# Kernel tuning notes

Measured on AMD Instinct MI355X. Metric: run time of the kernel, lower is better.

The kernel has to match this reference:

```python
import jax, jax.numpy as jnp
import numpy as np

N, E, D, H, LAYERS = 50000, 800000, 128, 8, 2
LRELU_ALPHA = 0.2


def _seg_softmax(logits, seg, n):
    # numerically stable softmax over edges grouped by destination node
    m = jax.ops.segment_max(logits, seg, num_segments=n)
    z = jnp.exp(logits - m[seg])
    s = jax.ops.segment_sum(z, seg, num_segments=n)
    return z / jnp.maximum(s[seg], 1e-16)


def _gat_layer(x, src, dst, W, a_src, a_dst, concat):
    # W: [H, Fin, F'], a_src/a_dst: [H, F']
    n = x.shape[0]
    outs = []
    for h in range(W.shape[0]):  # loop over heads to bound peak memory
        Wh = x @ W[h]                              # [N, F']
        es = Wh @ a_src[h]                         # [N]
        ed = Wh @ a_dst[h]                         # [N]
        e = jax.nn.leaky_relu(es[src] + ed[dst], LRELU_ALPHA)  # [E]
        att = _seg_softmax(e, dst, n)              # [E]
        out = jax.ops.segment_sum(att[:, None] * Wh[src], dst, num_segments=n)
        outs.append(out)
    if concat:
        return jax.nn.elu(jnp.concatenate(outs, axis=-1))  # [N, H*F']
    return jnp.mean(jnp.stack(outs, axis=0), axis=0)        # [N, F']


def _rel_gcn_layer(x, src, dst, w, W):
    # weighted-adjacency GCN with row (in-degree) normalization + ReLU
    n = x.shape[0]
    deg = jax.ops.segment_sum(w, dst, num_segments=n)
    norm = w / jnp.maximum(deg[dst], 1e-16)        # [E]
    h = x @ W                                      # [N, Dout]
    agg = jax.ops.segment_sum(norm[:, None] * h[src], dst, num_segments=n)
    return jax.nn.relu(agg)


def setup_inputs() -> dict:
    key = jax.random.key(0)
    ks = jax.random.split(key, 12)
    s = 1.0 / np.sqrt(D)
    return {
        "x": jax.random.normal(ks[0], (N, D), dtype=jnp.float32),
        "edge_index": jax.random.randint(ks[1], (2, E), 0, N, dtype=jnp.int64),
        "edge_weight": jax.random.uniform(ks[2], (E,), dtype=jnp.float32),
        "gat_W0": jax.random.normal(ks[3], (H, D, D // H), dtype=jnp.float32) * s,
        "gat_a0_src": jax.random.normal(ks[4], (H, D // H), dtype=jnp.float32) * s,
        "gat_a0_dst": jax.random.normal(ks[5], (H, D // H), dtype=jnp.float32) * s,
        "gat_W1": jax.random.normal(ks[6], (H, D, D), dtype=jnp.float32) * s,
        "gat_a1_src": jax.random.normal(ks[7], (H, D), dtype=jnp.float32) * s,
        "gat_a1_dst": jax.random.normal(ks[8], (H, D), dtype=jnp.float32) * s,
        "gcn_W0": jax.random.normal(ks[9], (D, D), dtype=jnp.float32) * s,
        "gcn_W1": jax.random.normal(ks[10], (D, D), dtype=jnp.float32) * s,
    }


def reference(x, edge_index, edge_weight, gat_W0, gat_a0_src, gat_a0_dst,
              gat_W1, gat_a1_src, gat_a1_dst, gcn_W0, gcn_W1):
    src, dst = edge_index[0], edge_index[1]
    gat_params = [(gat_W0, gat_a0_src, gat_a0_dst), (gat_W1, gat_a1_src, gat_a1_dst)]
    gcn_params = [gcn_W0, gcn_W1]
    x1, x2 = x, x  # dropout is identity in eval mode
    for i in range(LAYERS):
        W, a_s, a_d = gat_params[i]
        x1 = _gat_layer(x1, src, dst, W, a_s, a_d, concat=(i != LAYERS - 1))
        x2 = _rel_gcn_layer(x2, src, dst, edge_weight, gcn_params[i])
    # cat along new last dim then MaxPool1d(2) == elementwise max of branches
    return jnp.maximum(x1, x2)
```

## Files before the change

kernel.cpp:

```cpp
#include <hip/hip_runtime.h>

#define LRELU_ALPHA 0.2f

typedef __attribute__((ext_vector_type(8))) short short8;
typedef __attribute__((ext_vector_type(4))) float float4v;
typedef __attribute__((ext_vector_type(2))) float f32x2;

__device__ __forceinline__ unsigned short f2bf(float f) {
  union { float f; unsigned u; } x; x.f = f;
  unsigned r = (x.u + 0x7fff + ((x.u >> 16) & 1)) >> 16;
  return (unsigned short)r;
}
__device__ __forceinline__ float bflo(unsigned u) {
  union { unsigned u; float f; } x; x.u = u << 16; return x.f;
}
__device__ __forceinline__ float bfhi(unsigned u) {
  union { unsigned u; float f; } x; x.u = u & 0xffff0000u; return x.f;
}
__device__ __forceinline__ f32x2 bfpair(unsigned u) {
  return (f32x2){bflo(u), bfhi(u)};
}


__global__ __launch_bounds__(256) void k_count(const int* __restrict__ dst,
                                               int* __restrict__ cnt, int E) {
  int e = blockIdx.x * 256 + threadIdx.x;
  if (e < E) atomicAdd(&cnt[dst[e]], 1);
}

__global__ __launch_bounds__(1024) void k_scan1(const int* __restrict__ cnt,
                                                int* __restrict__ lscan,
                                                int* __restrict__ bsum, int N) {
  __shared__ int sm[1024];
  int t = threadIdx.x;
  int base = blockIdx.x * 1024;
  int v = (base + t < N) ? cnt[base + t] : 0;
  sm[t] = v;
  __syncthreads();
  for (int off = 1; off < 1024; off <<= 1) {
    int x = (t >= off) ? sm[t - off] : 0;
    __syncthreads();
    sm[t] += x;
    __syncthreads();
  }
  if (base + t < N) lscan[base + t] = sm[t] - v;
  if (t == 1023) bsum[blockIdx.x] = sm[1023];
}

__global__ __launch_bounds__(64) void k_scan2(int* __restrict__ bsum,
                                              int* __restrict__ rowptrN, int nb) {
  int t = threadIdx.x;
  int v = (t < nb) ? bsum[t] : 0;
  int orig = v;
  for (int off = 1; off < 64; off <<= 1) {
    int y = __shfl_up(v, off, 64);
    if (t >= off) v += y;
  }
  if (t < nb) bsum[t] = v - orig;
  if (t == 63) *rowptrN = v;
}

__global__ __launch_bounds__(1024) void k_scan3(int* __restrict__ rowptr,
                                                int* __restrict__ cur,
                                                const int* __restrict__ bsum, int N) {
  int i = blockIdx.x * 1024 + threadIdx.x;
  if (i < N) {
    int v = rowptr[i] + bsum[blockIdx.x];
    rowptr[i] = v;
    cur[i] = v;
  }
}

__global__ __launch_bounds__(256) void k_scatter(const int* __restrict__ src,
                                                 const int* __restrict__ dst,
                                                 const float* __restrict__ w,
                                                 int* __restrict__ cur,
                                                 uint2* __restrict__ edata, int E) {
  int e = blockIdx.x * 256 + threadIdx.x;
  if (e < E) {
    int d = dst[e];
    int p = atomicAdd(&cur[d], 1);
    edata[p] = make_uint2((unsigned)src[e], __float_as_uint(w[e]));
  }
}

__global__ __launch_bounds__(256) void k_pack(const float* __restrict__ W0,
                                              const float* __restrict__ a0s,
                                              const float* __restrict__ a0d,
                                              const float* __restrict__ W1,
                                              const float* __restrict__ a1s,
                                              const float* __restrict__ a1d,
                                              const float* __restrict__ gw0,
                                              const float* __restrict__ gw1,
                                              unsigned short* __restrict__ W0catT,
                                              float* __restrict__ logitW,
                                              unsigned short* __restrict__ gw1T,
                                              unsigned short* __restrict__ va1T,
                                              unsigned short* __restrict__ WstackT) {
  int idx = blockIdx.x * 256 + threadIdx.x;
  if (idx < 32768) {
    int n = idx >> 7, k = idx & 127;
    int q = n >> 2, r = n & 3;
    float v;
    if (r < 2) {
      int o = 2 * q + r;
      int h = o >> 4, f = o & 15;
      v = W0[h * 2048 + k * 16 + f];
    } else {
      int j = 2 * q + (r - 2);
      v = gw0[k * 128 + j];
    }
    W0catT[idx] = f2bf(v);
  } else if (idx < 34816) {
    int j = idx - 32768;
    int k = j >> 4, c = j & 15;
    int h = (c < 8) ? c : c - 8;
    const float* a = (c < 8) ? a0s : a0d;
    float s = 0.f;
    for (int f = 0; f < 16; ++f) s += W0[h * 2048 + k * 16 + f] * a[h * 16 + f];
    logitW[j] = s;
  } else if (idx < 51200) {
    int j = idx - 34816;
    int n = j >> 7, k = j & 127;
    gw1T[j] = f2bf(gw1[k * 128 + n]);
  } else if (idx < 53248) {
    int j = idx - 51200;
    int c = j >> 7, k = j & 127;
    int h = c & 7;
    const float* a = (c < 8) ? a1s : a1d;
    float s = 0.f;
    for (int f = 0; f < 128; ++f) s += W1[h * 16384 + k * 128 + f] * a[h * 128 + f];
    va1T[j] = f2bf(s);
  } else if (idx < 184320) {
    int j = idx - 53248;
    int n = j >> 10, kk = j & 1023;
    int h = kk >> 7, k = kk & 127;
    WstackT[j] = f2bf(W1[h * 16384 + k * 128 + n] * 0.125f);
  }
}

__global__ __launch_bounds__(256) void k_prep(const float* __restrict__ x,
                                              const float* __restrict__ logitW,
                                              unsigned short* __restrict__ xb,
                                              float* __restrict__ logit0, int N) {
  __shared__ float sm[16][132];
  __shared__ float sw[2048];
  int t = threadIdx.x;
  int base = blockIdx.x * 16;
  int r = t >> 4, cc = (t & 15) * 8;
  const float* xr = x + (size_t)(base + r) * 128 + cc;
  float4 v0 = *(const float4*)xr;
  float4 v1 = *(const float4*)(xr + 4);
  ushort4 o0 = {f2bf(v0.x), f2bf(v0.y), f2bf(v0.z), f2bf(v0.w)};
  ushort4 o1 = {f2bf(v1.x), f2bf(v1.y), f2bf(v1.z), f2bf(v1.w)};
  *(ushort4*)(xb + (size_t)(base + r) * 128 + cc) = o0;
  *(ushort4*)(xb + (size_t)(base + r) * 128 + cc + 4) = o1;
  *(float4*)&sm[r][cc] = v0;
  *(float4*)&sm[r][cc + 4] = v1;
  *(float4*)&sw[t * 8] = *(const float4*)(logitW + t * 8);
  *(float4*)&sw[t * 8 + 4] = *(const float4*)(logitW + t * 8 + 4);
  __syncthreads();
  int c = t & 15;
  float acc = 0.f;
#pragma unroll
  for (int k = 0; k < 128; ++k) acc += sm[r][k] * sw[k * 16 + c];
  logit0[(size_t)(base + r) * 16 + c] = acc;
}

template <int NT, int OUT_BF16, int EPI>
__global__ __launch_bounds__(256) void k_mgemm(const unsigned short* __restrict__ A, int lda,
                                               const unsigned short* __restrict__ BT, int ldb,
                                               void* __restrict__ Cv, int ldc,
                                               const void* __restrict__ aux,
                                               int M, int Ncols, int K) {
  __shared__ unsigned short As[64][64];
  __shared__ unsigned short Bs[NT * 16][64];
  int tid = threadIdx.x;
  int w = tid >> 6, lane = tid & 63;
  int quad = lane >> 4, l16 = lane & 15;
  int row0 = blockIdx.x * 64;
  int c0 = blockIdx.y * (NT * 16);
  float4v acc[NT];
#pragma unroll
  for (int t = 0; t < NT; ++t) acc[t] = (float4v){0.f, 0.f, 0.f, 0.f};

  for (int k0 = 0; k0 < K; k0 += 64) {
    __syncthreads();
#pragma unroll
    for (int i = 0; i < 2; ++i) {
      int c = tid + i * 256;
      int r = c >> 3, kc = c & 7;
      uint4 v = {0u, 0u, 0u, 0u};
      int gr = row0 + r;
      if (gr < M) v = *(const uint4*)(A + (size_t)gr * lda + k0 + kc * 8);
      *(uint4*)(&As[r][(kc ^ (r & 7)) * 8]) = v;
    }
#pragma unroll
    for (int i = 0; i < (NT * 128 + 255) / 256; ++i) {
      int c = tid + i * 256;
      if (c < NT * 128) {
        int n = c >> 3, kc = c & 7;
        uint4 v = {0u, 0u, 0u, 0u};
        int gn = c0 + n;
        if (gn < Ncols) v = *(const uint4*)(BT + (size_t)gn * ldb + k0 + kc * 8);
        *(uint4*)(&Bs[n][(kc ^ (n & 7)) * 8]) = v;
      }
    }
    __syncthreads();
#pragma unroll
    for (int ks = 0; ks < 2; ++ks) {
      int m = w * 16 + l16;
      int ga = (ks * 4 + quad) ^ (m & 7);
      short8 a = *(const short8*)(&As[m][ga * 8]);
#pragma unroll
      for (int t = 0; t < NT; ++t) {
        int n = t * 16 + l16;
        int gb = (ks * 4 + quad) ^ (n & 7);
        short8 b = *(const short8*)(&Bs[n][gb * 8]);
        acc[t] = __builtin_amdgcn_mfma_f32_16x16x32_bf16(a, b, acc[t], 0, 0, 0);
      }
    }
  }
#pragma unroll
  for (int t = 0; t < NT; ++t) {
    int cc = c0 + t * 16 + l16;
    if (cc >= Ncols) continue;
#pragma unroll
    for (int i = 0; i < 4; ++i) {
      int rr = row0 + w * 16 + quad * 4 + i;
      if (rr >= M) continue;
      float v = acc[t][i];
      if (EPI == 1) {
        unsigned short us = ((const unsigned short*)aux)[(size_t)rr * ldc + cc];
        v = fmaxf(v, bflo((unsigned)us));
      }
      if (EPI == 2) {
        ((unsigned short*)Cv)[(size_t)rr * 256 + 4 * (cc >> 1) + 2 + (cc & 1)] = f2bf(v);
      } else if (OUT_BF16)
        ((unsigned short*)Cv)[(size_t)rr * ldc + cc] = f2bf(v);
      else
        ((float*)Cv)[(size_t)rr * ldc + cc] = v;
    }
  }
}

__global__ __launch_bounds__(256) void k_agg0(const unsigned short* __restrict__ feat0i,
                                              const float* __restrict__ logit0,
                                              const int* __restrict__ rowptr,
                                              const uint2* __restrict__ edata,
                                              unsigned short* __restrict__ x1c,
                                              unsigned short* __restrict__ x2,
                                              unsigned short* __restrict__ xh, int N) {
  __shared__ uint2 swl[4][64];
  int wave = threadIdx.x >> 6, lane = threadIdx.x & 63;
  int d = blockIdx.x * 4 + wave;
  if (d >= N) return;
  int head = lane >> 3, hh = lane & 7, j8 = lane >> 3;
  float edv = logit0[(size_t)d * 16 + 8 + hh];
  int beg = rowptr[d], end = rowptr[d + 1], deg = end - beg;
  float l = 0.f, wsum = 0.f;
  f32x2 a2 = {0.f, 0.f}, g2 = {0.f, 0.f};
  for (int base = 0; base < deg; base += 64) {
    int idx = beg + base + lane;
    uint2 sv = make_uint2(0u, 0u);
    if (idx < end) sv = edata[idx];
    swl[wave][lane] = sv;
    int ng = deg - base; if (ng > 64) ng = 64;
    int groups = (ng + 7) >> 3;
    for (int g = 0; g < groups; ++g) {
      uint2 swj = swl[wave][g * 8 + j8];
      float es = logit0[(size_t)swj.x * 16 + hh];
      float lg = es + edv;
      lg = lg > 0.f ? lg : LRELU_ALPHA * lg;
      float pme = __expf(fminf(lg, 80.f));
      if (g * 8 + j8 >= ng) pme = 0.f;
#pragma unroll
      for (int j = 0; j < 8; ++j) {
        uint2 sw = swl[wave][g * 8 + j];
        float pj = __shfl(pme, j * 8 + head, 64);
        float wj = __uint_as_float(sw.y);
        uint2 u = *(const uint2*)(feat0i + (size_t)sw.x * 256 + 4 * lane);
        a2 += bfpair(u.x) * pj;
        g2 += bfpair(u.y) * wj;
        l += pj;
        wsum += wj;
      }
    }
  }
  float inv = l > 0.f ? 1.f / l : 0.f;
  float v0 = a2.x * inv, v1 = a2.y * inv;
  v0 = v0 > 0.f ? v0 : __expf(v0) - 1.f;
  v1 = v1 > 0.f ? v1 : __expf(v1) - 1.f;
  unsigned xpack = (unsigned)f2bf(v0) | ((unsigned)f2bf(v1) << 16);
  ((unsigned*)x1c)[(size_t)d * 64 + lane] = xpack;
  ((unsigned*)xh)[(size_t)d * 128 + 2 * lane] = xpack;
  float ginv = 1.f / fmaxf(wsum, 1e-16f);
  float w0 = fmaxf(g2.x * ginv, 0.f), w1 = fmaxf(g2.y * ginv, 0.f);
  ((unsigned*)x2)[(size_t)d * 64 + lane] = (unsigned)f2bf(w0) | ((unsigned)f2bf(w1) << 16);
}

__global__ __launch_bounds__(256) void k_agg1(const unsigned short* __restrict__ xh,
                                              const float* __restrict__ esed,
                                              const int* __restrict__ rowptr,
                                              const uint2* __restrict__ edata,
                                              unsigned short* __restrict__ aggbuf,
                                              unsigned short* __restrict__ x2f,
                                              int d0, int d1) {
  __shared__ uint2 swl[4][64];
  __shared__ float pl[4][64];
  int wave = threadIdx.x >> 6, lane = threadIdx.x & 63;
  int d = d0 + blockIdx.x * 4 + wave;
  if (d >= d1) return;
  int hh = lane & 7, j8 = lane >> 3;
  float ed = esed[(size_t)d * 16 + 8 + hh];
  int beg = rowptr[d], end = rowptr[d + 1], deg = end - beg;
  f32x2 ax2[8] = {};
  f32x2 g2 = {0.f, 0.f};
  float lpart = 0.f, wsum = 0.f;
  for (int base = 0; base < deg; base += 64) {
    int idx = beg + base + lane;
    uint2 sv = make_uint2(0u, 0u);
    if (idx < end) sv = edata[idx];
    swl[wave][lane] = sv;
    int ng = deg - base; if (ng > 64) ng = 64;
    int groups = (ng + 7) >> 3;
    for (int g = 0; g < groups; ++g) {
      uint2 swj = swl[wave][g * 8 + j8];
      float es = esed[(size_t)swj.x * 16 + hh];
      float lg = es + ed;
      lg = lg > 0.f ? lg : LRELU_ALPHA * lg;
      float pme = __expf(fminf(lg, 80.f));
      if (g * 8 + j8 >= ng) pme = 0.f;
      lpart += pme;
      pl[wave][lane] = pme;
#pragma unroll
      for (int j = 0; j < 8; ++j) {
        uint2 sw = swl[wave][g * 8 + j];
        float4 pv0 = *(const float4*)&pl[wave][j * 8];
        float4 pv1 = *(const float4*)&pl[wave][j * 8 + 4];
        uint2 u = *(const uint2*)(xh + (size_t)sw.x * 256 + 4 * lane);
        f32x2 xv = bfpair(u.x);
        float wj = __uint_as_float(sw.y);
        g2 += bfpair(u.y) * wj;
        wsum += wj;
        ax2[0] += xv * pv0.x;
        ax2[1] += xv * pv0.y;
        ax2[2] += xv * pv0.z;
        ax2[3] += xv * pv0.w;
        ax2[4] += xv * pv1.x;
        ax2[5] += xv * pv1.y;
        ax2[6] += xv * pv1.z;
        ax2[7] += xv * pv1.w;
      }
    }
  }
  lpart += __shfl_xor(lpart, 8, 64);
  lpart += __shfl_xor(lpart, 16, 64);
  lpart += __shfl_xor(lpart, 32, 64);
  size_t lr = (size_t)(d - d0) * 512;
#pragma unroll
  for (int h = 0; h < 8; ++h) {
    float lh = __shfl(lpart, h, 64);
    float inv = lh > 0.f ? 1.f / lh : 0.f;
    ((unsigned*)aggbuf)[lr + h * 64 + lane] =
        (unsigned)f2bf(ax2[h].x * inv) | ((unsigned)f2bf(ax2[h].y * inv) << 16);
  }
  float ginv = 1.f / fmaxf(wsum, 1e-16f);
  float w0 = fmaxf(g2.x * ginv, 0.f), w1 = fmaxf(g2.y * ginv, 0.f);
  ((unsigned*)x2f)[(size_t)d * 64 + lane] = (unsigned)f2bf(w0) | ((unsigned)f2bf(w1) << 16);
}


extern "C" void kernel_launch(void* const* d_in, const int* in_sizes, int n_in,
                              void* d_out, int out_size, void* d_ws, size_t ws_size,
                              hipStream_t stream) {
  const float* x   = (const float*)d_in[0];
  const int*   ei  = (const int*)d_in[1];
  const float* ew  = (const float*)d_in[2];
  const float* W0  = (const float*)d_in[3];
  const float* a0s = (const float*)d_in[4];
  const float* a0d = (const float*)d_in[5];
  const float* W1  = (const float*)d_in[6];
  const float* a1s = (const float*)d_in[7];
  const float* a1d = (const float*)d_in[8];
  const float* gw0 = (const float*)d_in[9];
  const float* gw1 = (const float*)d_in[10];
  float* out = (float*)d_out;

  const int N = in_sizes[0] / 128;
  const int E = in_sizes[1] / 2;
  const int* src = ei;
  const int* dst = ei + E;

  char* p = (char*)d_ws;
  auto carve = [&](size_t bytes) {
    void* r = (void*)p;
    p += (bytes + 255) & ~(size_t)255;
    return r;
  };
  int*   cnt    = (int*)carve((size_t)N * 4);
  int*   rowptr = (int*)carve((size_t)(N + 1) * 4);
  int*   cur    = (int*)carve((size_t)N * 4);
  int*   bsum   = (int*)carve(256 * 4);
  uint2* edata  = (uint2*)carve((size_t)E * 8);
  unsigned short* W0catT  = (unsigned short*)carve(32768 * 2);
  float*          logitW  = (float*)carve(2048 * 4);
  unsigned short* gw1T    = (unsigned short*)carve(16384 * 2);
  unsigned short* va1T    = (unsigned short*)carve(2048 * 2);
  unsigned short* WstackT = (unsigned short*)carve(131072 * 2);
  unsigned short* x1c  = (unsigned short*)carve((size_t)N * 128 * 2);
  unsigned short* x2   = (unsigned short*)carve((size_t)N * 128 * 2);
  unsigned short* x2f  = (unsigned short*)carve((size_t)N * 128 * 2);
  float*          esed = (float*)carve((size_t)N * 16 * 4);
  unsigned short* xh   = (unsigned short*)carve((size_t)N * 256 * 2);
  const int CH = 25600;
  size_t ph1 = ((size_t)N * 128 * 2 + 255) & ~(size_t)255;
  size_t ph2 = ph1 + (((size_t)N * 256 * 2 + 255) & ~(size_t)255);
  size_t ph3 = ph2 + (((size_t)N * 16 * 4 + 255) & ~(size_t)255);
  size_t scratch_sz = (size_t)CH * 1024 * 2;
  if (ph3 > scratch_sz) scratch_sz = ph3;
  char* scratch = (char*)carve(scratch_sz);
  unsigned short* xb     = (unsigned short*)scratch;
  unsigned short* feat0i = (unsigned short*)(scratch + ph1);
  float*          logit0 = (float*)(scratch + ph2);
  unsigned short* aggbuf = (unsigned short*)scratch;

  hipMemsetAsync(cnt, 0, (size_t)N * 4, stream);
  int gE = (E + 255) / 256;
  k_count<<<gE, 256, 0, stream>>>(dst, cnt, E);
  int nb = (N + 1023) / 1024;
  k_scan1<<<nb, 1024, 0, stream>>>(cnt, rowptr, bsum, N);
  k_scan2<<<1, 64, 0, stream>>>(bsum, rowptr + N, nb);
  k_scan3<<<nb, 1024, 0, stream>>>(rowptr, cur, bsum, N);
  k_scatter<<<gE, 256, 0, stream>>>(src, dst, ew, cur, edata, E);

  k_pack<<<(184320 + 255) / 256, 256, 0, stream>>>(W0, a0s, a0d, W1, a1s, a1d, gw0,
                                                   gw1, W0catT, logitW, gw1T, va1T,
                                                   WstackT);
  k_prep<<<(N + 15) / 16, 256, 0, stream>>>(x, logitW, xb, logit0, N);

  int gM = (N + 63) / 64;
  k_mgemm<8, 1, 0><<<dim3(gM, 2), 256, 0, stream>>>(xb, 128, W0catT, 128, feat0i, 256,
                                                    nullptr, N, 256, 128);
  k_agg0<<<(N + 3) / 4, 256, 0, stream>>>(feat0i, logit0, rowptr, edata,
                                          x1c, x2, xh, N);

  k_mgemm<1, 0, 0><<<dim3(gM, 1), 256, 0, stream>>>(x1c, 128, va1T, 128, esed, 16,
                                                    nullptr, N, 16, 128);
  k_mgemm<8, 1, 2><<<dim3(gM, 1), 256, 0, stream>>>(x2, 128, gw1T, 128, xh, 256,
                                                    nullptr, N, 128, 128);

  for (int d0 = 0; d0 < N; d0 += CH) {
    int d1 = d0 + CH < N ? d0 + CH : N;
    int chN = d1 - d0;
    k_agg1<<<(chN + 3) / 4, 256, 0, stream>>>(xh, esed, rowptr, edata,
                                              aggbuf, x2f, d0, d1);
    k_mgemm<8, 0, 1><<<dim3((chN + 63) / 64, 1), 256, 0, stream>>>(
        aggbuf, 1024, WstackT, 1024, out + (size_t)d0 * 128, 128,
        x2f + (size_t)d0 * 128, chN, 128, 1024);
  }
}
```

Before: 488.0 us.

## Precompute per-edge attention weights and softmax normalizers in separate edge kernel

Result: slower. 502.7 us (+3.0%).

```diff
diff --git a/kernel.cpp b/kernel.cpp
--- a/kernel.cpp
+++ b/kernel.cpp
@@ -167,6 +167,33 @@
   logit0[(size_t)(base + r) * 16 + c] = acc;
 }
 
+__global__ __launch_bounds__(256) void k_pedge(const float* __restrict__ logits,
+                                               const uint2* __restrict__ edata,
+                                               const int* __restrict__ rowptr,
+                                               unsigned short* __restrict__ pedge,
+                                               float* __restrict__ linv, int N) {
+  int wave = threadIdx.x >> 6, lane = threadIdx.x & 63;
+  int d = blockIdx.x * 4 + wave;
+  if (d >= N) return;
+  int j8 = lane >> 3, h = lane & 7;
+  float edv = logits[(size_t)d * 16 + 8 + h];
+  int beg = rowptr[d], end = rowptr[d + 1];
+  float lsum = 0.f;
+  for (int ii = beg + j8; ii < end; ii += 8) {
+    unsigned s = edata[ii].x;
+    float es = logits[(size_t)s * 16 + h];
+    float lg = es + edv;
+    lg = lg > 0.f ? lg : LRELU_ALPHA * lg;
+    float p = __expf(fminf(lg, 80.f));
+    lsum += p;
+    pedge[(size_t)ii * 8 + h] = f2bf(p);
+  }
+  lsum += __shfl_xor(lsum, 8, 64);
+  lsum += __shfl_xor(lsum, 16, 64);
+  lsum += __shfl_xor(lsum, 32, 64);
+  if (lane < 8) linv[(size_t)d * 8 + h] = lsum > 0.f ? 1.f / lsum : 0.f;
+}
+
 template <int NT, int OUT_BF16, int EPI>
 __global__ __launch_bounds__(256) void k_mgemm(const unsigned short* __restrict__ A, int lda,
                                                const unsigned short* __restrict__ BT, int ldb,
@@ -245,49 +272,54 @@
 }
 
 __global__ __launch_bounds__(256) void k_agg0(const unsigned short* __restrict__ feat0i,
-                                              const float* __restrict__ logit0,
                                               const int* __restrict__ rowptr,
                                               const uint2* __restrict__ edata,
+                                              const unsigned short* __restrict__ pedge,
+                                              const float* __restrict__ linv,
                                               unsigned short* __restrict__ x1c,
                                               unsigned short* __restrict__ x2,
                                               unsigned short* __restrict__ xh, int N) {
   __shared__ uint2 swl[4][64];
+  __shared__ float pl[4][512];
   int wave = threadIdx.x >> 6, lane = threadIdx.x & 63;
   int d = blockIdx.x * 4 + wave;
   if (d >= N) return;
-  int head = lane >> 3, hh = lane & 7, j8 = lane >> 3;
-  float edv = logit0[(size_t)d * 16 + 8 + hh];
+  int head = lane >> 3;
   int beg = rowptr[d], end = rowptr[d + 1], deg = end - beg;
-  float l = 0.f, wsum = 0.f;
+  float wsum = 0.f;
   f32x2 a2 = {0.f, 0.f}, g2 = {0.f, 0.f};
   for (int base = 0; base < deg; base += 64) {
     int idx = beg + base + lane;
+    bool valid = idx < end;
     uint2 sv = make_uint2(0u, 0u);
-    if (idx < end) sv = edata[idx];
+    float4 pa = {0.f, 0.f, 0.f, 0.f}, pb = {0.f, 0.f, 0.f, 0.f};
+    if (valid) {
+      sv = edata[idx];
+      ushort4 q0 = *(const ushort4*)(pedge + (size_t)idx * 8);
+      ushort4 q1 = *(const ushort4*)(pedge + (size_t)idx * 8 + 4);
+      pa = make_float4(bflo(q0.x), bflo(q0.y), bflo(q0.z), bflo(q0.w));
+      pb = make_float4(bflo(q1.x), bflo(q1.y), bflo(q1.z), bflo(q1.w));
+    }
     swl[wave][lane] = sv;
+    *(float4*)&pl[wave][lane * 8] = pa;
+    *(float4*)&pl[wave][lane * 8 + 4] = pb;
     int ng = deg - base; if (ng > 64) ng = 64;
     int groups = (ng + 7) >> 3;
     for (int g = 0; g < groups; ++g) {
-      uint2 swj = swl[wave][g * 8 + j8];
-      float es = logit0[(size_t)swj.x * 16 + hh];
-      float lg = es + edv;
-      lg = lg > 0.f ? lg : LRELU_ALPHA * lg;
-      float pme = __expf(fminf(lg, 80.f));
-      if (g * 8 + j8 >= ng) pme = 0.f;
 #pragma unroll
       for (int j = 0; j < 8; ++j) {
-        uint2 sw = swl[wave][g * 8 + j];
-        float pj = __shfl(pme, j * 8 + head, 64);
+        int e = g * 8 + j;
+        uint2 sw = swl[wave][e];
+        float pj = pl[wave][e * 8 + head];
         float wj = __uint_as_float(sw.y);
         uint2 u = *(const uint2*)(feat0i + (size_t)sw.x * 256 + 4 * lane);
         a2 += bfpair(u.x) * pj;
         g2 += bfpair(u.y) * wj;
-        l += pj;
         wsum += wj;
       }
     }
   }
-  float inv = l > 0.f ? 1.f / l : 0.f;
+  float inv = linv[(size_t)d * 8 + head];
   float v0 = a2.x * inv, v1 = a2.y * inv;
   v0 = v0 > 0.f ? v0 : __expf(v0) - 1.f;
   v1 = v1 > 0.f ? v1 : __expf(v1) - 1.f;
@@ -300,44 +332,46 @@
 }
 
 __global__ __launch_bounds__(256) void k_agg1(const unsigned short* __restrict__ xh,
-                                              const float* __restrict__ esed,
                                               const int* __restrict__ rowptr,
                                               const uint2* __restrict__ edata,
+                                              const unsigned short* __restrict__ pedge,
+                                              const float* __restrict__ linv,
                                               unsigned short* __restrict__ aggbuf,
                                               unsigned short* __restrict__ x2f,
                                               int d0, int d1) {
   __shared__ uint2 swl[4][64];
-  __shared__ float pl[4][64];
+  __shared__ float pl[4][512];
   int wave = threadIdx.x >> 6, lane = threadIdx.x & 63;
   int d = d0 + blockIdx.x * 4 + wave;
   if (d >= d1) return;
-  int hh = lane & 7, j8 = lane >> 3;
-  float ed = esed[(size_t)d * 16 + 8 + hh];
   int beg = rowptr[d], end = rowptr[d + 1], deg = end - beg;
   f32x2 ax2[8] = {};
   f32x2 g2 = {0.f, 0.f};
-  float lpart = 0.f, wsum = 0.f;
+  float wsum = 0.f;
   for (int base = 0; base < deg; base += 64) {
     int idx = beg + base + lane;
+    bool valid = idx < end;
     uint2 sv = make_uint2(0u, 0u);
-    if (idx < end) sv = edata[idx];
+    float4 pa = {0.f, 0.f, 0.f, 0.f}, pb = {0.f, 0.f, 0.f, 0.f};
+    if (valid) {
+      sv = edata[idx];
+      ushort4 q0 = *(const ushort4*)(pedge + (size_t)idx * 8);
+      ushort4 q1 = *(const ushort4*)(pedge + (size_t)idx * 8 + 4);
+      pa = make_float4(bflo(q0.x), bflo(q0.y), bflo(q0.z), bflo(q0.w));
+      pb = make_float4(bflo(q1.x), bflo(q1.y), bflo(q1.z), bflo(q1.w));
+    }
     swl[wave][lane] = sv;
+    *(float4*)&pl[wave][lane * 8] = pa;
+    *(float4*)&pl[wave][lane * 8 + 4] = pb;
     int ng = deg - base; if (ng > 64) ng = 64;
     int groups = (ng + 7) >> 3;
     for (int g = 0; g < groups; ++g) {
-      uint2 swj = swl[wave][g * 8 + j8];
-      float es = esed[(size_t)swj.x * 16 + hh];
-      float lg = es + ed;
-      lg = lg > 0.f ? lg : LRELU_ALPHA * lg;
-      float pme = __expf(fminf(lg, 80.f));
-      if (g * 8 + j8 >= ng) pme = 0.f;
-      lpart += pme;
-      pl[wave][lane] = pme;
 #pragma unroll
       for (int j = 0; j < 8; ++j) {
-        uint2 sw = swl[wave][g * 8 + j];
-        float4 pv0 = *(const float4*)&pl[wave][j * 8];
-        float4 pv1 = *(const float4*)&pl[wave][j * 8 + 4];
+        int e = g * 8 + j;
+        uint2 sw = swl[wave][e];
+        float4 pv0 = *(const float4*)&pl[wave][e * 8];
+        float4 pv1 = *(const float4*)&pl[wave][e * 8 + 4];
         uint2 u = *(const uint2*)(xh + (size_t)sw.x * 256 + 4 * lane);
         f32x2 xv = bfpair(u.x);
         float wj = __uint_as_float(sw.y);
@@ -354,16 +388,14 @@
       }
     }
   }
-  lpart += __shfl_xor(lpart, 8, 64);
-  lpart += __shfl_xor(lpart, 16, 64);
-  lpart += __shfl_xor(lpart, 32, 64);
+  float4 i0 = *(const float4*)(linv + (size_t)d * 8);
+  float4 i1 = *(const float4*)(linv + (size_t)d * 8 + 4);
+  float invh[8] = {i0.x, i0.y, i0.z, i0.w, i1.x, i1.y, i1.z, i1.w};
   size_t lr = (size_t)(d - d0) * 512;
 #pragma unroll
   for (int h = 0; h < 8; ++h) {
-    float lh = __shfl(lpart, h, 64);
-    float inv = lh > 0.f ? 1.f / lh : 0.f;
     ((unsigned*)aggbuf)[lr + h * 64 + lane] =
-        (unsigned)f2bf(ax2[h].x * inv) | ((unsigned)f2bf(ax2[h].y * inv) << 16);
+        (unsigned)f2bf(ax2[h].x * invh[h]) | ((unsigned)f2bf(ax2[h].y * invh[h]) << 16);
   }
   float ginv = 1.f / fmaxf(wsum, 1e-16f);
   float w0 = fmaxf(g2.x * ginv, 0.f), w1 = fmaxf(g2.y * ginv, 0.f);
@@ -413,6 +445,9 @@
   unsigned short* x2f  = (unsigned short*)carve((size_t)N * 128 * 2);
   float*          esed = (float*)carve((size_t)N * 16 * 4);
   unsigned short* xh   = (unsigned short*)carve((size_t)N * 256 * 2);
+  unsigned short* pedge = (unsigned short*)carve((size_t)E * 8 * 2);
+  float*          linv0 = (float*)carve((size_t)N * 8 * 4);
+  float*          linv1 = (float*)carve((size_t)N * 8 * 4);
   const int CH = 25600;
   size_t ph1 = ((size_t)N * 128 * 2 + 255) & ~(size_t)255;
   size_t ph2 = ph1 + (((size_t)N * 256 * 2 + 255) & ~(size_t)255);
@@ -440,20 +475,23 @@
   k_prep<<<(N + 15) / 16, 256, 0, stream>>>(x, logitW, xb, logit0, N);
 
   int gM = (N + 63) / 64;
+  int gD = (N + 3) / 4;
   k_mgemm<8, 1, 0><<<dim3(gM, 2), 256, 0, stream>>>(xb, 128, W0catT, 128, feat0i, 256,
                                                     nullptr, N, 256, 128);
-  k_agg0<<<(N + 3) / 4, 256, 0, stream>>>(feat0i, logit0, rowptr, edata,
-                                          x1c, x2, xh, N);
+  k_pedge<<<gD, 256, 0, stream>>>(logit0, edata, rowptr, pedge, linv0, N);
+  k_agg0<<<gD, 256, 0, stream>>>(feat0i, rowptr, edata, pedge, linv0, x1c, x2, xh, N);
 
   k_mgemm<1, 0, 0><<<dim3(gM, 1), 256, 0, stream>>>(x1c, 128, va1T, 128, esed, 16,
                                                     nullptr, N, 16, 128);
   k_mgemm<8, 1, 2><<<dim3(gM, 1), 256, 0, stream>>>(x2, 128, gw1T, 128, xh, 256,
                                                     nullptr, N, 128, 128);
 
+  k_pedge<<<gD, 256, 0, stream>>>(esed, edata, rowptr, pedge, linv1, N);
+
   for (int d0 = 0; d0 < N; d0 += CH) {
     int d1 = d0 + CH < N ? d0 + CH : N;
     int chN = d1 - d0;
-    k_agg1<<<(chN + 3) / 4, 256, 0, stream>>>(xh, esed, rowptr, edata,
+    k_agg1<<<(chN + 3) / 4, 256, 0, stream>>>(xh, rowptr, edata, pedge, linv1,
                                               aggbuf, x2f, d0, d1);
     k_mgemm<8, 0, 1><<<dim3((chN + 63) / 64, 1), 256, 0, stream>>>(
         aggbuf, 1024, WstackT, 1024, out + (size_t)d0 * 128, 128,
```
